# Performance work log

Measured on AMD Instinct MI355X. Metric: run time of the kernel, lower is better.

The kernel has to match this reference:

```python
import jax, jax.numpy as jnp
import numpy as np

N_NODES = 75000
N_EDGES = 1200000


def gcn_conv(x, src, dst, W, b, n):
    # linear transform first (PyG GCNConv applies lin before propagate)
    h = x @ W  # [n, out]
    # add self loops
    loop = jnp.arange(n, dtype=src.dtype)
    s = jnp.concatenate([src, loop])
    d = jnp.concatenate([dst, loop])
    # symmetric normalization: deg computed on destination after self-loops
    deg = jnp.zeros((n,), dtype=h.dtype).at[d].add(1.0)
    dinv = jnp.where(deg > 0, jax.lax.rsqrt(deg), 0.0)
    norm = dinv[s] * dinv[d]  # [E+n]
    msgs = h[s] * norm[:, None]  # gather + scale, [E+n, out]
    out = jax.ops.segment_sum(msgs, d, num_segments=n)  # scatter-add
    return out + b


def setup_inputs() -> dict:
    key = jax.random.key(0)
    ks = jax.random.split(key, 6)
    x = jax.random.normal(ks[0], (N_NODES, 64), dtype=jnp.float32)
    edge_index = jax.random.randint(ks[1], (2, N_EDGES), 0, N_NODES, dtype=jnp.int64)
    # Glorot-ish scaled weights
    W1 = jax.random.normal(ks[2], (64, 64), dtype=jnp.float32) * (1.0 / np.sqrt(64))
    b1 = jax.random.normal(ks[3], (64,), dtype=jnp.float32) * 0.01
    W2 = jax.random.normal(ks[4], (64, 16), dtype=jnp.float32) * (1.0 / np.sqrt(64))
    b2 = jax.random.normal(ks[5], (16,), dtype=jnp.float32) * 0.01
    return {"x": x, "edge_index": edge_index, "W1": W1, "b1": b1, "W2": W2, "b2": b2}


def reference(x, edge_index, W1, b1, W2, b2):
    src, dst = edge_index[0], edge_index[1]
    h = gcn_conv(x, src, dst, W1, b1, N_NODES)
    h = jax.nn.relu(h)
    # dropout is identity in eval mode
    out = gcn_conv(h, src, dst, W2, b2, N_NODES)
    return out
```

## Files before the change

kernel.cpp:

```cpp
#include <hip/hip_runtime.h>


#define NBSHIFT 9
#define BUCKET_NODES 512
#define CAP 10240
#define CHA 8192
#define TA 512
#define TB 512
#define MAXNB 160
#define EPT 16

__device__ __forceinline__ unsigned bfpack(float a, float b) {
  unsigned ua = __float_as_uint(a), ub = __float_as_uint(b);
  ua += 0x7fffu + ((ua >> 16) & 1u);
  ub += 0x7fffu + ((ub >> 16) & 1u);
  return (ua >> 16) | (ub & 0xffff0000u);
}
__device__ __forceinline__ float bflo(unsigned u) { return __uint_as_float(u << 16); }
__device__ __forceinline__ float bfhi(unsigned u) { return __uint_as_float(u & 0xffff0000u); }

__launch_bounds__(TA)
__global__ void kA_bucket(const int* __restrict__ src, const int* __restrict__ dst,
                          int* __restrict__ bucketCur, int* __restrict__ bucketArr,
                          int NB, int E) {
  __shared__ int stage[CHA];
  __shared__ unsigned char binOf[CHA];
  __shared__ int cnt[MAXNB];
  __shared__ int off[MAXNB];
  __shared__ int gpos[MAXNB];
  __shared__ int cursor[MAXNB];
  __shared__ int scanbuf[256];
  int t = threadIdx.x;
  int e0 = blockIdx.x * CHA;

  for (int i = t; i < NB; i += TA) cnt[i] = 0;
  __syncthreads();
  int dreg[EPT];
  #pragma unroll
  for (int j = 0; j < EPT; j++) {
    int e = e0 + t + j * TA;
    dreg[j] = (e < E) ? dst[e] : -1;
    if (dreg[j] >= 0) atomicAdd(&cnt[dreg[j] >> NBSHIFT], 1);
  }
  __syncthreads();
  if (t < 256) scanbuf[t] = (t < NB) ? cnt[t] : 0;
  __syncthreads();
  for (int o = 1; o < 256; o <<= 1) {
    int add = (t < 256 && t >= o) ? scanbuf[t - o] : 0;
    __syncthreads();
    if (t < 256) scanbuf[t] += add;
    __syncthreads();
  }
  if (t < NB) {
    off[t] = scanbuf[t] - cnt[t];
    cursor[t] = off[t];
    gpos[t] = (cnt[t] > 0) ? atomicAdd(&bucketCur[t], cnt[t]) : 0;
  }
  __syncthreads();
  #pragma unroll
  for (int j = 0; j < EPT; j++) {
    int e = e0 + t + j * TA;
    if (dreg[j] >= 0) {
      int d = dreg[j], s = src[e];
      int b = d >> NBSHIFT;
      int p = atomicAdd(&cursor[b], 1);
      stage[p] = (s << NBSHIFT) | (d & (BUCKET_NODES - 1));
      binOf[p] = (unsigned char)b;
    }
  }
  __syncthreads();
  int total = scanbuf[255];
  for (int i = t; i < total; i += TA) {
    int b = binOf[i];
    int destIdx = gpos[b] + (i - off[b]);
    if (destIdx < CAP) bucketArr[b * CAP + destIdx] = stage[i];
  }
}

__launch_bounds__(TB)
__global__ void kB_fill(const int* __restrict__ bucketArr, const int* __restrict__ bucketCur,
                        int* __restrict__ rp, float* __restrict__ dinv,
                        int* __restrict__ col, int N, int NB) {
  __shared__ int cnts[MAXNB];
  __shared__ int hist[BUCKET_NODES];
  __shared__ int cur[BUCKET_NODES];
  __shared__ int wsum[8], woff[8];
  __shared__ int s_base;
  int b = blockIdx.x;
  int t = threadIdx.x;
  int nE = min(bucketCur[b], CAP);
  int base = b * CAP;

  if (t < NB) cnts[t] = min(bucketCur[t], CAP);
  hist[t] = 0;
  __syncthreads();
  for (int i = t; i < nE; i += TB)
    atomicAdd(&hist[bucketArr[base + i] & (BUCKET_NODES - 1)], 1);
  __syncthreads();
  int myv = hist[t];
  int lane = t & 63, w = t >> 6;
  int incl = myv;
  #pragma unroll
  for (int o = 1; o < 64; o <<= 1) {
    int v = __shfl_up(incl, o);
    if (lane >= o) incl += v;
  }
  if (lane == 63) wsum[w] = incl;
  __syncthreads();
  if (t == 0) {
    int acc = 0;
    for (int i = 0; i < b; i++) acc += cnts[i];
    s_base = acc;
    int a2 = 0;
    #pragma unroll
    for (int i = 0; i < 8; i++) { woff[i] = a2; a2 += wsum[i]; }
    if (b == NB - 1) rp[N] = acc + nE;
  }
  __syncthreads();
  int gexcl = s_base + woff[w] + (incl - myv);
  cur[t] = gexcl;
  int gnode = b * BUCKET_NODES + t;
  if (gnode < N) {
    rp[gnode] = gexcl;
    dinv[gnode] = rsqrtf((float)(myv + 1));
  }
  __syncthreads();
  for (int i = t; i < nE; i += TB) {
    int v = bucketArr[base + i];
    int p = atomicAdd(&cur[v & (BUCKET_NODES - 1)], 1);
    col[p] = v >> NBSHIFT;
  }
}

__launch_bounds__(256)
__global__ void k_gemm64(const float4* __restrict__ X4, const float4* __restrict__ W4,
                         const float* __restrict__ dinv, uint2* __restrict__ outb,
                         int n) {
  __shared__ float4 Xs[64 * 17];
  __shared__ float4 Ws[64 * 16];
  int t = threadIdx.x;
  int base = blockIdx.x * 64;
  {
    int rr = t >> 2, q = t & 3;
    int r = base + rr;
    #pragma unroll
    for (int c = 0; c < 4; c++) {
      float4 v = make_float4(0.f, 0.f, 0.f, 0.f);
      if (r < n) v = X4[r * 16 + q * 4 + c];
      Xs[rr * 17 + q * 4 + c] = v;
      Ws[t + 256 * c] = W4[t + 256 * c];
    }
  }
  __syncthreads();

  int tx = t & 15, ty = t >> 4;
  float4 a0 = make_float4(0.f, 0.f, 0.f, 0.f), a1 = a0, a2 = a0, a3 = a0;
  #pragma unroll
  for (int kb = 0; kb < 16; kb++) {
    float4 x0 = Xs[(ty * 4 + 0) * 17 + kb];
    float4 x1 = Xs[(ty * 4 + 1) * 17 + kb];
    float4 x2 = Xs[(ty * 4 + 2) * 17 + kb];
    float4 x3 = Xs[(ty * 4 + 3) * 17 + kb];
    float4 w0 = Ws[(kb * 4 + 0) * 16 + tx];
    float4 w1 = Ws[(kb * 4 + 1) * 16 + tx];
    float4 w2 = Ws[(kb * 4 + 2) * 16 + tx];
    float4 w3 = Ws[(kb * 4 + 3) * 16 + tx];
    #define FMA4(A, XS) \
      A.x = fmaf(XS.x, w0.x, A.x); A.y = fmaf(XS.x, w0.y, A.y); \
      A.z = fmaf(XS.x, w0.z, A.z); A.w = fmaf(XS.x, w0.w, A.w); \
      A.x = fmaf(XS.y, w1.x, A.x); A.y = fmaf(XS.y, w1.y, A.y); \
      A.z = fmaf(XS.y, w1.z, A.z); A.w = fmaf(XS.y, w1.w, A.w); \
      A.x = fmaf(XS.z, w2.x, A.x); A.y = fmaf(XS.z, w2.y, A.y); \
      A.z = fmaf(XS.z, w2.z, A.z); A.w = fmaf(XS.z, w2.w, A.w); \
      A.x = fmaf(XS.w, w3.x, A.x); A.y = fmaf(XS.w, w3.y, A.y); \
      A.z = fmaf(XS.w, w3.z, A.z); A.w = fmaf(XS.w, w3.w, A.w);
    FMA4(a0, x0) FMA4(a1, x1) FMA4(a2, x2) FMA4(a3, x3)
    #undef FMA4
  }
  #pragma unroll
  for (int i = 0; i < 4; i++) {
    int r = base + ty * 4 + i;
    if (r < n) {
      float s = dinv[r];
      float4 a = (i == 0) ? a0 : (i == 1) ? a1 : (i == 2) ? a2 : a3;
      uint2 pk;
      pk.x = bfpack(a.x * s, a.y * s);
      pk.y = bfpack(a.z * s, a.w * s);
      outb[r * 16 + tx] = pk;
    }
  }
}

__launch_bounds__(256)
__global__ void k_agg64(const uint2* __restrict__ hsb,
                        const int* __restrict__ rp,
                        const int* __restrict__ col,
                        const float* __restrict__ dinv,
                        const float* __restrict__ b1,
                        uint2* __restrict__ h1b,
                        int n) {
  int lane = threadIdx.x & 63;
  int c = lane & 15;
  int node = ((blockIdx.x * blockDim.x + threadIdx.x) >> 6) * 4 + (lane >> 4);
  if (node >= n) return;

  float4 b14 = ((const float4*)b1)[c];
  int s0 = rp[node], s1 = rp[node + 1];
  int dt = s1 - s0 + 1;
  float ax = 0.f, ay = 0.f, az = 0.f, aw = 0.f;
  int t = 0;
  int i0 = 0, i1 = 0, i2 = 0, i3 = 0, i4 = 0, i5 = 0, i6 = 0, i7 = 0;
  i0 = node;
  if (1 < dt) i1 = col[s0 + 0];
  if (2 < dt) i2 = col[s0 + 1];
  if (3 < dt) i3 = col[s0 + 2];
  if (4 < dt) i4 = col[s0 + 3];
  if (5 < dt) i5 = col[s0 + 4];
  if (6 < dt) i6 = col[s0 + 5];
  if (7 < dt) i7 = col[s0 + 6];
  while (t < dt) {
    int c0 = i0, c1 = i1, c2 = i2, c3 = i3, c4 = i4, c5 = i5, c6 = i6, c7 = i7;
    bool h1_ = (t + 1) < dt, h2_ = (t + 2) < dt, h3_ = (t + 3) < dt;
    bool h4_ = (t + 4) < dt, h5_ = (t + 5) < dt, h6_ = (t + 6) < dt;
    bool h7_ = (t + 7) < dt;
    int tn = t + 8;
    if (tn + 0 < dt) i0 = col[s0 + tn - 1];
    if (tn + 1 < dt) i1 = col[s0 + tn + 0];
    if (tn + 2 < dt) i2 = col[s0 + tn + 1];
    if (tn + 3 < dt) i3 = col[s0 + tn + 2];
    if (tn + 4 < dt) i4 = col[s0 + tn + 3];
    if (tn + 5 < dt) i5 = col[s0 + tn + 4];
    if (tn + 6 < dt) i6 = col[s0 + tn + 5];
    if (tn + 7 < dt) i7 = col[s0 + tn + 6];
    uint2 u0 = hsb[c0 * 16 + c];
    uint2 u1 = h1_ ? hsb[c1 * 16 + c] : make_uint2(0u, 0u);
    uint2 u2 = h2_ ? hsb[c2 * 16 + c] : make_uint2(0u, 0u);
    uint2 u3 = h3_ ? hsb[c3 * 16 + c] : make_uint2(0u, 0u);
    uint2 u4 = h4_ ? hsb[c4 * 16 + c] : make_uint2(0u, 0u);
    uint2 u5 = h5_ ? hsb[c5 * 16 + c] : make_uint2(0u, 0u);
    uint2 u6 = h6_ ? hsb[c6 * 16 + c] : make_uint2(0u, 0u);
    uint2 u7 = h7_ ? hsb[c7 * 16 + c] : make_uint2(0u, 0u);
    #define ACC(U) \
      ax += bflo(U.x); ay += bfhi(U.x); az += bflo(U.y); aw += bfhi(U.y);
    ACC(u0) ACC(u1) ACC(u2) ACC(u3) ACC(u4) ACC(u5) ACC(u6) ACC(u7)
    #undef ACC
    t = tn;
  }
  float dv = dinv[node];
  uint2 pk;
  pk.x = bfpack(fmaxf(ax * dv + b14.x, 0.f), fmaxf(ay * dv + b14.y, 0.f));
  pk.y = bfpack(fmaxf(az * dv + b14.z, 0.f), fmaxf(aw * dv + b14.w, 0.f));
  h1b[node * 16 + c] = pk;
}

__launch_bounds__(256)
__global__ void k_gemmB(const uint2* __restrict__ h1b,
                        const float4* __restrict__ W24,
                        const float* __restrict__ dinv,
                        unsigned* __restrict__ hs2b,
                        int n) {
  __shared__ float4 Ws[256];
  int t = threadIdx.x;
  Ws[t] = W24[t];
  __syncthreads();
  int tx = t & 3, ty = t >> 2;
  int r0 = blockIdx.x * 256 + ty * 4;
  float4 a0 = make_float4(0.f, 0.f, 0.f, 0.f), a1 = a0, a2 = a0, a3 = a0;
  #pragma unroll
  for (int q = 0; q < 16; q++) {
    uint2 u0 = (r0 + 0 < n) ? h1b[(r0 + 0) * 16 + q] : make_uint2(0u, 0u);
    uint2 u1 = (r0 + 1 < n) ? h1b[(r0 + 1) * 16 + q] : make_uint2(0u, 0u);
    uint2 u2 = (r0 + 2 < n) ? h1b[(r0 + 2) * 16 + q] : make_uint2(0u, 0u);
    uint2 u3 = (r0 + 3 < n) ? h1b[(r0 + 3) * 16 + q] : make_uint2(0u, 0u);
    #pragma unroll
    for (int kk = 0; kk < 4; kk++) {
      float4 w = Ws[(4 * q + kk) * 4 + tx];
      float v0 = (kk == 0) ? bflo(u0.x) : (kk == 1) ? bfhi(u0.x) : (kk == 2) ? bflo(u0.y) : bfhi(u0.y);
      float v1 = (kk == 0) ? bflo(u1.x) : (kk == 1) ? bfhi(u1.x) : (kk == 2) ? bflo(u1.y) : bfhi(u1.y);
      float v2 = (kk == 0) ? bflo(u2.x) : (kk == 1) ? bfhi(u2.x) : (kk == 2) ? bflo(u2.y) : bfhi(u2.y);
      float v3 = (kk == 0) ? bflo(u3.x) : (kk == 1) ? bfhi(u3.x) : (kk == 2) ? bflo(u3.y) : bfhi(u3.y);
      a0.x = fmaf(v0, w.x, a0.x); a0.y = fmaf(v0, w.y, a0.y);
      a0.z = fmaf(v0, w.z, a0.z); a0.w = fmaf(v0, w.w, a0.w);
      a1.x = fmaf(v1, w.x, a1.x); a1.y = fmaf(v1, w.y, a1.y);
      a1.z = fmaf(v1, w.z, a1.z); a1.w = fmaf(v1, w.w, a1.w);
      a2.x = fmaf(v2, w.x, a2.x); a2.y = fmaf(v2, w.y, a2.y);
      a2.z = fmaf(v2, w.z, a2.z); a2.w = fmaf(v2, w.w, a2.w);
      a3.x = fmaf(v3, w.x, a3.x); a3.y = fmaf(v3, w.y, a3.y);
      a3.z = fmaf(v3, w.z, a3.z); a3.w = fmaf(v3, w.w, a3.w);
    }
  }
  #pragma unroll
  for (int i = 0; i < 4; i++) {
    int r = r0 + i;
    if (r < n) {
      float dv = dinv[r];
      float4 a = (i == 0) ? a0 : (i == 1) ? a1 : (i == 2) ? a2 : a3;
      hs2b[r * 8 + 2 * tx]     = bfpack(a.x * dv, a.y * dv);
      hs2b[r * 8 + 2 * tx + 1] = bfpack(a.z * dv, a.w * dv);
    }
  }
}

__launch_bounds__(256)
__global__ void k_agg16(const uint2* __restrict__ hs2b,
                        const int* __restrict__ rp,
                        const int* __restrict__ col,
                        const float* __restrict__ dinv,
                        const float* __restrict__ b2,
                        float4* __restrict__ out4,
                        int n) {
  int lane = threadIdx.x & 63;
  int hl = lane & 7;
  int c = hl & 3;
  int sub = hl >> 2;
  int node = ((blockIdx.x * blockDim.x + threadIdx.x) >> 6) * 8 + (lane >> 3);
  if (node >= n) return;

  int s0 = rp[node], s1 = rp[node + 1];
  int dt = s1 - s0 + 1;
  float ax = 0.f, ay = 0.f, az = 0.f, aw = 0.f;
  int t = sub;
  int i0 = 0, i1 = 0, i2 = 0, i3 = 0;
  if (t < dt)     i0 = (t == 0) ? node : col[s0 + t - 1];
  if (t + 2 < dt) i1 = col[s0 + t + 1];
  if (t + 4 < dt) i2 = col[s0 + t + 3];
  if (t + 6 < dt) i3 = col[s0 + t + 5];
  while (t < dt) {
    int c0 = i0, c1 = i1, c2 = i2, c3 = i3;
    bool h1_ = (t + 2) < dt, h2_ = (t + 4) < dt, h3_ = (t + 6) < dt;
    int tn = t + 8;
    if (tn < dt)     i0 = col[s0 + tn - 1];
    if (tn + 2 < dt) i1 = col[s0 + tn + 1];
    if (tn + 4 < dt) i2 = col[s0 + tn + 3];
    if (tn + 6 < dt) i3 = col[s0 + tn + 5];
    uint2 u0 = hs2b[c0 * 4 + c];
    uint2 u1 = h1_ ? hs2b[c1 * 4 + c] : make_uint2(0u, 0u);
    uint2 u2 = h2_ ? hs2b[c2 * 4 + c] : make_uint2(0u, 0u);
    uint2 u3 = h3_ ? hs2b[c3 * 4 + c] : make_uint2(0u, 0u);
    ax += bflo(u0.x) + bflo(u1.x) + bflo(u2.x) + bflo(u3.x);
    ay += bfhi(u0.x) + bfhi(u1.x) + bfhi(u2.x) + bfhi(u3.x);
    az += bflo(u0.y) + bflo(u1.y) + bflo(u2.y) + bflo(u3.y);
    aw += bfhi(u0.y) + bfhi(u1.y) + bfhi(u2.y) + bfhi(u3.y);
    t = tn;
  }
  ax += __shfl_xor(ax, 4);
  ay += __shfl_xor(ay, 4);
  az += __shfl_xor(az, 4);
  aw += __shfl_xor(aw, 4);
  if (sub == 0) {
    float dv = dinv[node];
    float4 b24 = ((const float4*)b2)[c];
    float4 o;
    o.x = ax * dv + b24.x;
    o.y = ay * dv + b24.y;
    o.z = az * dv + b24.z;
    o.w = aw * dv + b24.w;
    out4[node * 4 + c] = o;
  }
}

extern "C" void kernel_launch(void* const* d_in, const int* in_sizes, int n_in,
                              void* d_out, int out_size, void* d_ws, size_t ws_size,
                              hipStream_t stream) {
  const float* x  = (const float*)d_in[0];
  const int* edges = (const int*)d_in[1];
  const float* W1 = (const float*)d_in[2];
  const float* b1 = (const float*)d_in[3];
  const float* W2 = (const float*)d_in[4];
  const float* b2 = (const float*)d_in[5];
  float* out = (float*)d_out;

  const int N = in_sizes[0] / 64;
  const int E = in_sizes[1] / 2;
  const int* src = edges;
  const int* dst = edges + E;
  const int NB = (N + BUCKET_NODES - 1) >> NBSHIFT;

  auto align = [](size_t v) { return (v + 255) & ~(size_t)255; };
  char* p = (char*)d_ws;
  float* dinv       = (float*)p; p += align((size_t)N * 4);
  int*   rp         = (int*)p;   p += align((size_t)(N + 1) * 4);
  int*   bucketCur  = (int*)p;   p += align((size_t)MAXNB * 4);
  int*   col        = (int*)p;   p += align((size_t)E * 4);
  float* hs1        = (float*)p; p += align((size_t)N * 64 * 4);
  float* h1b        = (float*)p; p += align((size_t)N * 64 * 2);
  float* hs2        = (float*)p; p += align((size_t)N * 16 * 2);
  int* bucketArr = (int*)hs1;

  const int nbA = (E + CHA - 1) / CHA;
  const int nbW4 = (int)((((size_t)(N + 3) / 4) * 64 + 255) / 256);
  const int nbW8 = (int)((((size_t)(N + 7) / 8) * 64 + 255) / 256);

  hipMemsetAsync(bucketCur, 0, (size_t)MAXNB * 4, stream);
  kA_bucket<<<nbA, TA, 0, stream>>>(src, dst, bucketCur, bucketArr, NB, E);
  kB_fill  <<<NB, TB, 0, stream>>>(bucketArr, bucketCur, rp, dinv, col, N, NB);

  k_gemm64<<<(N + 63) / 64, 256, 0, stream>>>((const float4*)x, (const float4*)W1,
                                              dinv, (uint2*)hs1, N);
  k_agg64 <<<nbW4, 256, 0, stream>>>((const uint2*)hs1, rp, col, dinv,
                                     b1, (uint2*)h1b, N);
  k_gemmB <<<(N + 255) / 256, 256, 0, stream>>>((const uint2*)h1b,
                                                (const float4*)W2, dinv,
                                                (unsigned*)hs2, N);
  k_agg16 <<<nbW8, 256, 0, stream>>>((const uint2*)hs2, rp, col, dinv,
                                     b2, (float4*)out, N);
}
```

Baseline: 120.5 us.

## Fuse bucketing with layer-1 GEMM and fold W2 GEMM into aggregation

The edge-bucketing kernel and the layer-1 dense transform now run as one launch with a block-index split, so the GEMM no longer depends on dinv and overlaps with graph construction. The source-side dinv scaling moves into the aggregation loop as a per-neighbor gather. The layer-2 GEMM is folded into the layer-1 aggregation via wavefront shuffles, which removes the h1 intermediate round trip and one launch. In exchange the aggregation does extra dinv gathers, bucketArr gets its own workspace region instead of aliasing hs1, and the unscaled bf16 h differs slightly in rounding.

After: 255.4 us. 112% more time.

```diff
diff --git a/kernel.cpp b/kernel.cpp
--- a/kernel.cpp
+++ b/kernel.cpp
@@ -19,61 +19,113 @@
 __device__ __forceinline__ float bflo(unsigned u) { return __uint_as_float(u << 16); }
 __device__ __forceinline__ float bfhi(unsigned u) { return __uint_as_float(u & 0xffff0000u); }
 
-__launch_bounds__(TA)
-__global__ void kA_bucket(const int* __restrict__ src, const int* __restrict__ dst,
-                          int* __restrict__ bucketCur, int* __restrict__ bucketArr,
-                          int NB, int E) {
-  __shared__ int stage[CHA];
-  __shared__ unsigned char binOf[CHA];
-  __shared__ int cnt[MAXNB];
-  __shared__ int off[MAXNB];
-  __shared__ int gpos[MAXNB];
-  __shared__ int cursor[MAXNB];
-  __shared__ int scanbuf[256];
+__launch_bounds__(512)
+__global__ void k_fused1(const int* __restrict__ srcp, const int* __restrict__ dstp,
+                         int* __restrict__ bucketCur, int* __restrict__ bucketArr,
+                         int NB, int E, int nbA,
+                         const float4* __restrict__ X4, const float4* __restrict__ W4,
+                         uint2* __restrict__ outb, int n) {
+  __shared__ __align__(16) char smem[44544];
   int t = threadIdx.x;
-  int e0 = blockIdx.x * CHA;
-
-  for (int i = t; i < NB; i += TA) cnt[i] = 0;
-  __syncthreads();
-  int dreg[EPT];
-  #pragma unroll
-  for (int j = 0; j < EPT; j++) {
-    int e = e0 + t + j * TA;
-    dreg[j] = (e < E) ? dst[e] : -1;
-    if (dreg[j] >= 0) atomicAdd(&cnt[dreg[j] >> NBSHIFT], 1);
-  }
-  __syncthreads();
-  if (t < 256) scanbuf[t] = (t < NB) ? cnt[t] : 0;
-  __syncthreads();
-  for (int o = 1; o < 256; o <<= 1) {
-    int add = (t < 256 && t >= o) ? scanbuf[t - o] : 0;
-    __syncthreads();
-    if (t < 256) scanbuf[t] += add;
-    __syncthreads();
-  }
-  if (t < NB) {
-    off[t] = scanbuf[t] - cnt[t];
-    cursor[t] = off[t];
-    gpos[t] = (cnt[t] > 0) ? atomicAdd(&bucketCur[t], cnt[t]) : 0;
-  }
-  __syncthreads();
-  #pragma unroll
-  for (int j = 0; j < EPT; j++) {
-    int e = e0 + t + j * TA;
-    if (dreg[j] >= 0) {
-      int d = dreg[j], s = src[e];
-      int b = d >> NBSHIFT;
-      int p = atomicAdd(&cursor[b], 1);
-      stage[p] = (s << NBSHIFT) | (d & (BUCKET_NODES - 1));
-      binOf[p] = (unsigned char)b;
-    }
-  }
-  __syncthreads();
-  int total = scanbuf[255];
-  for (int i = t; i < total; i += TA) {
-    int b = binOf[i];
-    int destIdx = gpos[b] + (i - off[b]);
-    if (destIdx < CAP) bucketArr[b * CAP + destIdx] = stage[i];
+  if ((int)blockIdx.x < nbA) {
+    int* stage = (int*)smem;
+    unsigned char* binOf = (unsigned char*)(smem + 32768);
+    int* cnt    = (int*)(smem + 40960);
+    int* off    = (int*)(smem + 41600);
+    int* gpos   = (int*)(smem + 42240);
+    int* cursor = (int*)(smem + 42880);
+    int* scanbuf= (int*)(smem + 43520);
+    int e0 = blockIdx.x * CHA;
+
+    for (int i = t; i < NB; i += TA) cnt[i] = 0;
+    __syncthreads();
+    int dreg[EPT];
+    #pragma unroll
+    for (int j = 0; j < EPT; j++) {
+      int e = e0 + t + j * TA;
+      dreg[j] = (e < E) ? dstp[e] : -1;
+      if (dreg[j] >= 0) atomicAdd(&cnt[dreg[j] >> NBSHIFT], 1);
+    }
+    __syncthreads();
+    if (t < 256) scanbuf[t] = (t < NB) ? cnt[t] : 0;
+    __syncthreads();
+    for (int o = 1; o < 256; o <<= 1) {
+      int add = (t < 256 && t >= o) ? scanbuf[t - o] : 0;
+      __syncthreads();
+      if (t < 256) scanbuf[t] += add;
+      __syncthreads();
+    }
+    if (t < NB) {
+      off[t] = scanbuf[t] - cnt[t];
+      cursor[t] = off[t];
+      gpos[t] = (cnt[t] > 0) ? atomicAdd(&bucketCur[t], cnt[t]) : 0;
+    }
+    __syncthreads();
+    #pragma unroll
+    for (int j = 0; j < EPT; j++) {
+      int e = e0 + t + j * TA;
+      if (dreg[j] >= 0) {
+        int d = dreg[j], s = srcp[e];
+        int b = d >> NBSHIFT;
+        int p = atomicAdd(&cursor[b], 1);
+        stage[p] = (s << NBSHIFT) | (d & (BUCKET_NODES - 1));
+        binOf[p] = (unsigned char)b;
+      }
+    }
+    __syncthreads();
+    int total = scanbuf[255];
+    for (int i = t; i < total; i += TA) {
+      int b = binOf[i];
+      int destIdx = gpos[b] + (i - off[b]);
+      if (destIdx < CAP) bucketArr[b * CAP + destIdx] = stage[i];
+    }
+  } else {
+    float4* Xs = (float4*)smem;
+    float4* Ws = (float4*)(smem + 17408);
+    int base = ((int)blockIdx.x - nbA) * 64;
+    {
+      int rr = t >> 3, q = t & 7;
+      int r = base + rr;
+      float4 z = make_float4(0.f, 0.f, 0.f, 0.f);
+      Xs[rr * 17 + q]     = (r < n) ? X4[r * 16 + q]     : z;
+      Xs[rr * 17 + q + 8] = (r < n) ? X4[r * 16 + q + 8] : z;
+      Ws[t]       = W4[t];
+      Ws[t + 512] = W4[t + 512];
+    }
+    __syncthreads();
+    int tx = t & 15, tyy = t >> 4;
+    float4 a0 = make_float4(0.f, 0.f, 0.f, 0.f), a1 = a0;
+    #pragma unroll
+    for (int kb = 0; kb < 16; kb++) {
+      float4 x0 = Xs[(tyy * 2 + 0) * 17 + kb];
+      float4 x1 = Xs[(tyy * 2 + 1) * 17 + kb];
+      float4 w0 = Ws[(kb * 4 + 0) * 16 + tx];
+      float4 w1 = Ws[(kb * 4 + 1) * 16 + tx];
+      float4 w2 = Ws[(kb * 4 + 2) * 16 + tx];
+      float4 w3 = Ws[(kb * 4 + 3) * 16 + tx];
+      #define FMA4(A, XS) \
+        A.x = fmaf(XS.x, w0.x, A.x); A.y = fmaf(XS.x, w0.y, A.y); \
+        A.z = fmaf(XS.x, w0.z, A.z); A.w = fmaf(XS.x, w0.w, A.w); \
+        A.x = fmaf(XS.y, w1.x, A.x); A.y = fmaf(XS.y, w1.y, A.y); \
+        A.z = fmaf(XS.y, w1.z, A.z); A.w = fmaf(XS.y, w1.w, A.w); \
+        A.x = fmaf(XS.z, w2.x, A.x); A.y = fmaf(XS.z, w2.y, A.y); \
+        A.z = fmaf(XS.z, w2.z, A.z); A.w = fmaf(XS.z, w2.w, A.w); \
+        A.x = fmaf(XS.w, w3.x, A.x); A.y = fmaf(XS.w, w3.y, A.y); \
+        A.z = fmaf(XS.w, w3.z, A.z); A.w = fmaf(XS.w, w3.w, A.w);
+      FMA4(a0, x0) FMA4(a1, x1)
+      #undef FMA4
+    }
+    #pragma unroll
+    for (int i = 0; i < 2; i++) {
+      int r = base + tyy * 2 + i;
+      if (r < n) {
+        float4 a = i ? a1 : a0;
+        uint2 pk;
+        pk.x = bfpack(a.x, a.y);
+        pk.y = bfpack(a.z, a.w);
+        outb[r * 16 + tx] = pk;
+      }
+    }
   }
 }
 
@@ -133,72 +185,17 @@
 }
 
 __launch_bounds__(256)
-__global__ void k_gemm64(const float4* __restrict__ X4, const float4* __restrict__ W4,
-                         const float* __restrict__ dinv, uint2* __restrict__ outb,
-                         int n) {
-  __shared__ float4 Xs[64 * 17];
-  __shared__ float4 Ws[64 * 16];
-  int t = threadIdx.x;
-  int base = blockIdx.x * 64;
-  {
-    int rr = t >> 2, q = t & 3;
-    int r = base + rr;
-    #pragma unroll
-    for (int c = 0; c < 4; c++) {
-      float4 v = make_float4(0.f, 0.f, 0.f, 0.f);
-      if (r < n) v = X4[r * 16 + q * 4 + c];
-      Xs[rr * 17 + q * 4 + c] = v;
-      Ws[t + 256 * c] = W4[t + 256 * c];
-    }
-  }
-  __syncthreads();
-
-  int tx = t & 15, ty = t >> 4;
-  float4 a0 = make_float4(0.f, 0.f, 0.f, 0.f), a1 = a0, a2 = a0, a3 = a0;
-  #pragma unroll
-  for (int kb = 0; kb < 16; kb++) {
-    float4 x0 = Xs[(ty * 4 + 0) * 17 + kb];
-    float4 x1 = Xs[(ty * 4 + 1) * 17 + kb];
-    float4 x2 = Xs[(ty * 4 + 2) * 17 + kb];
-    float4 x3 = Xs[(ty * 4 + 3) * 17 + kb];
-    float4 w0 = Ws[(kb * 4 + 0) * 16 + tx];
-    float4 w1 = Ws[(kb * 4 + 1) * 16 + tx];
-    float4 w2 = Ws[(kb * 4 + 2) * 16 + tx];
-    float4 w3 = Ws[(kb * 4 + 3) * 16 + tx];
-    #define FMA4(A, XS) \
-      A.x = fmaf(XS.x, w0.x, A.x); A.y = fmaf(XS.x, w0.y, A.y); \
-      A.z = fmaf(XS.x, w0.z, A.z); A.w = fmaf(XS.x, w0.w, A.w); \
-      A.x = fmaf(XS.y, w1.x, A.x); A.y = fmaf(XS.y, w1.y, A.y); \
-      A.z = fmaf(XS.y, w1.z, A.z); A.w = fmaf(XS.y, w1.w, A.w); \
-      A.x = fmaf(XS.z, w2.x, A.x); A.y = fmaf(XS.z, w2.y, A.y); \
-      A.z = fmaf(XS.z, w2.z, A.z); A.w = fmaf(XS.z, w2.w, A.w); \
-      A.x = fmaf(XS.w, w3.x, A.x); A.y = fmaf(XS.w, w3.y, A.y); \
-      A.z = fmaf(XS.w, w3.z, A.z); A.w = fmaf(XS.w, w3.w, A.w);
-    FMA4(a0, x0) FMA4(a1, x1) FMA4(a2, x2) FMA4(a3, x3)
-    #undef FMA4
-  }
-  #pragma unroll
-  for (int i = 0; i < 4; i++) {
-    int r = base + ty * 4 + i;
-    if (r < n) {
-      float s = dinv[r];
-      float4 a = (i == 0) ? a0 : (i == 1) ? a1 : (i == 2) ? a2 : a3;
-      uint2 pk;
-      pk.x = bfpack(a.x * s, a.y * s);
-      pk.y = bfpack(a.z * s, a.w * s);
-      outb[r * 16 + tx] = pk;
-    }
-  }
-}
-
-__launch_bounds__(256)
-__global__ void k_agg64(const uint2* __restrict__ hsb,
+__global__ void k_aggW2(const uint2* __restrict__ hsb,
                         const int* __restrict__ rp,
                         const int* __restrict__ col,
                         const float* __restrict__ dinv,
                         const float* __restrict__ b1,
-                        uint2* __restrict__ h1b,
+                        const float* __restrict__ W2,
+                        unsigned* __restrict__ hs2b,
                         int n) {
+  __shared__ float W2s[1024];
+  for (int i = threadIdx.x; i < 1024; i += 256) W2s[i] = W2[i];
+  __syncthreads();
   int lane = threadIdx.x & 63;
   int c = lane & 15;
   int node = ((blockIdx.x * blockDim.x + threadIdx.x) >> 6) * 4 + (lane >> 4);
@@ -209,8 +206,7 @@
   int dt = s1 - s0 + 1;
   float ax = 0.f, ay = 0.f, az = 0.f, aw = 0.f;
   int t = 0;
-  int i0 = 0, i1 = 0, i2 = 0, i3 = 0, i4 = 0, i5 = 0, i6 = 0, i7 = 0;
-  i0 = node;
+  int i0 = node, i1 = 0, i2 = 0, i3 = 0, i4 = 0, i5 = 0, i6 = 0, i7 = 0;
   if (1 < dt) i1 = col[s0 + 0];
   if (2 < dt) i2 = col[s0 + 1];
   if (3 < dt) i3 = col[s0 + 2];
@@ -232,6 +228,8 @@
     if (tn + 5 < dt) i5 = col[s0 + tn + 4];
     if (tn + 6 < dt) i6 = col[s0 + tn + 5];
     if (tn + 7 < dt) i7 = col[s0 + tn + 6];
+    float d0 = dinv[c0], d1 = dinv[c1], d2 = dinv[c2], d3 = dinv[c3];
+    float d4 = dinv[c4], d5 = dinv[c5], d6 = dinv[c6], d7 = dinv[c7];
     uint2 u0 = hsb[c0 * 16 + c];
     uint2 u1 = h1_ ? hsb[c1 * 16 + c] : make_uint2(0u, 0u);
     uint2 u2 = h2_ ? hsb[c2 * 16 + c] : make_uint2(0u, 0u);
@@ -240,65 +238,37 @@
     uint2 u5 = h5_ ? hsb[c5 * 16 + c] : make_uint2(0u, 0u);
     uint2 u6 = h6_ ? hsb[c6 * 16 + c] : make_uint2(0u, 0u);
     uint2 u7 = h7_ ? hsb[c7 * 16 + c] : make_uint2(0u, 0u);
-    #define ACC(U) \
-      ax += bflo(U.x); ay += bfhi(U.x); az += bflo(U.y); aw += bfhi(U.y);
-    ACC(u0) ACC(u1) ACC(u2) ACC(u3) ACC(u4) ACC(u5) ACC(u6) ACC(u7)
+    #define ACC(U, D) \
+      ax = fmaf(D, bflo(U.x), ax); ay = fmaf(D, bfhi(U.x), ay); \
+      az = fmaf(D, bflo(U.y), az); aw = fmaf(D, bfhi(U.y), aw);
+    ACC(u0, d0) ACC(u1, d1) ACC(u2, d2) ACC(u3, d3)
+    ACC(u4, d4) ACC(u5, d5) ACC(u6, d6) ACC(u7, d7)
     #undef ACC
     t = tn;
   }
   float dv = dinv[node];
-  uint2 pk;
-  pk.x = bfpack(fmaxf(ax * dv + b14.x, 0.f), fmaxf(ay * dv + b14.y, 0.f));
-  pk.y = bfpack(fmaxf(az * dv + b14.z, 0.f), fmaxf(aw * dv + b14.w, 0.f));
-  h1b[node * 16 + c] = pk;
-}
-
-__launch_bounds__(256)
-__global__ void k_gemmB(const uint2* __restrict__ h1b,
-                        const float4* __restrict__ W24,
-                        const float* __restrict__ dinv,
-                        unsigned* __restrict__ hs2b,
-                        int n) {
-  __shared__ float4 Ws[256];
-  int t = threadIdx.x;
-  Ws[t] = W24[t];
-  __syncthreads();
-  int tx = t & 3, ty = t >> 2;
-  int r0 = blockIdx.x * 256 + ty * 4;
-  float4 a0 = make_float4(0.f, 0.f, 0.f, 0.f), a1 = a0, a2 = a0, a3 = a0;
+  float h0  = fmaxf(ax * dv + b14.x, 0.f);
+  float h1v = fmaxf(ay * dv + b14.y, 0.f);
+  float h2v = fmaxf(az * dv + b14.z, 0.f);
+  float h3v = fmaxf(aw * dv + b14.w, 0.f);
+
+  float val = 0.f;
+  int gb = lane & 48;
   #pragma unroll
-  for (int q = 0; q < 16; q++) {
-    uint2 u0 = (r0 + 0 < n) ? h1b[(r0 + 0) * 16 + q] : make_uint2(0u, 0u);
-    uint2 u1 = (r0 + 1 < n) ? h1b[(r0 + 1) * 16 + q] : make_uint2(0u, 0u);
-    uint2 u2 = (r0 + 2 < n) ? h1b[(r0 + 2) * 16 + q] : make_uint2(0u, 0u);
-    uint2 u3 = (r0 + 3 < n) ? h1b[(r0 + 3) * 16 + q] : make_uint2(0u, 0u);
-    #pragma unroll
-    for (int kk = 0; kk < 4; kk++) {
-      float4 w = Ws[(4 * q + kk) * 4 + tx];
-      float v0 = (kk == 0) ? bflo(u0.x) : (kk == 1) ? bfhi(u0.x) : (kk == 2) ? bflo(u0.y) : bfhi(u0.y);
-      float v1 = (kk == 0) ? bflo(u1.x) : (kk == 1) ? bfhi(u1.x) : (kk == 2) ? bflo(u1.y) : bfhi(u1.y);
-      float v2 = (kk == 0) ? bflo(u2.x) : (kk == 1) ? bfhi(u2.x) : (kk == 2) ? bflo(u2.y) : bfhi(u2.y);
-      float v3 = (kk == 0) ? bflo(u3.x) : (kk == 1) ? bfhi(u3.x) : (kk == 2) ? bflo(u3.y) : bfhi(u3.y);
-      a0.x = fmaf(v0, w.x, a0.x); a0.y = fmaf(v0, w.y, a0.y);
-      a0.z = fmaf(v0, w.z, a0.z); a0.w = fmaf(v0, w.w, a0.w);
-      a1.x = fmaf(v1, w.x, a1.x); a1.y = fmaf(v1, w.y, a1.y);
-      a1.z = fmaf(v1, w.z, a1.z); a1.w = fmaf(v1, w.w, a1.w);
-      a2.x = fmaf(v2, w.x, a2.x); a2.y = fmaf(v2, w.y, a2.y);
-      a2.z = fmaf(v2, w.z, a2.z); a2.w = fmaf(v2, w.w, a2.w);
-      a3.x = fmaf(v3, w.x, a3.x); a3.y = fmaf(v3, w.y, a3.y);
-      a3.z = fmaf(v3, w.z, a3.z); a3.w = fmaf(v3, w.w, a3.w);
-    }
-  }
-  #pragma unroll
-  for (int i = 0; i < 4; i++) {
-    int r = r0 + i;
-    if (r < n) {
-      float dv = dinv[r];
-      float4 a = (i == 0) ? a0 : (i == 1) ? a1 : (i == 2) ? a2 : a3;
-      hs2b[r * 8 + 2 * tx]     = bfpack(a.x * dv, a.y * dv);
-      hs2b[r * 8 + 2 * tx + 1] = bfpack(a.z * dv, a.w * dv);
-    }
-  }
+  for (int kq = 0; kq < 16; kq++) {
+    int srcl = gb + kq;
+    float v0 = __shfl(h0, srcl);
+    float v1 = __shfl(h1v, srcl);
+    float v2 = __shfl(h2v, srcl);
+    float v3 = __shfl(h3v, srcl);
+    val = fmaf(v0, W2s[(4 * kq + 0) * 16 + c], val);
+    val = fmaf(v1, W2s[(4 * kq + 1) * 16 + c], val);
+    val = fmaf(v2, W2s[(4 * kq + 2) * 16 + c], val);
+    val = fmaf(v3, W2s[(4 * kq + 3) * 16 + c], val);
+  }
+  val *= dv;
+  float vnext = __shfl_down(val, 1);
+  if ((c & 1) == 0) hs2b[node * 8 + (c >> 1)] = bfpack(val, vnext);
 }
 
 __launch_bounds__(256)
@@ -382,26 +352,23 @@
   int*   rp         = (int*)p;   p += align((size_t)(N + 1) * 4);
   int*   bucketCur  = (int*)p;   p += align((size_t)MAXNB * 4);
   int*   col        = (int*)p;   p += align((size_t)E * 4);
-  float* hs1        = (float*)p; p += align((size_t)N * 64 * 4);
-  float* h1b        = (float*)p; p += align((size_t)N * 64 * 2);
+  int*   bucketArr  = (int*)p;   p += align((size_t)MAXNB * CAP * 4);
+  float* hs1        = (float*)p; p += align((size_t)N * 64 * 2);
   float* hs2        = (float*)p; p += align((size_t)N * 16 * 2);
-  int* bucketArr = (int*)hs1;
 
   const int nbA = (E + CHA - 1) / CHA;
+  const int ngemm = (N + 63) / 64;
   const int nbW4 = (int)((((size_t)(N + 3) / 4) * 64 + 255) / 256);
   const int nbW8 = (int)((((size_t)(N + 7) / 8) * 64 + 255) / 256);
 
   hipMemsetAsync(bucketCur, 0, (size_t)MAXNB * 4, stream);
-  kA_bucket<<<nbA, TA, 0, stream>>>(src, dst, bucketCur, bucketArr, NB, E);
-  kB_fill  <<<NB, TB, 0, stream>>>(bucketArr, bucketCur, rp, dinv, col, N, NB);
-
-  k_gemm64<<<(N + 63) / 64, 256, 0, stream>>>((const float4*)x, (const float4*)W1,
-                                              dinv, (uint2*)hs1, N);
-  k_agg64 <<<nbW4, 256, 0, stream>>>((const uint2*)hs1, rp, col, dinv,
-                                     b1, (uint2*)h1b, N);
-  k_gemmB <<<(N + 255) / 256, 256, 0, stream>>>((const uint2*)h1b,
-                                                (const float4*)W2, dinv,
-                                                (unsigned*)hs2, N);
-  k_agg16 <<<nbW8, 256, 0, stream>>>((const uint2*)hs2, rp, col, dinv,
-                                     b2, (float4*)out, N);
-}
+  k_fused1<<<nbA + ngemm, 512, 0, stream>>>(src, dst, bucketCur, bucketArr,
+                                            NB, E, nbA,
+                                            (const float4*)x, (const float4*)W1,
+                                            (uint2*)hs1, N);
+  kB_fill<<<NB, TB, 0, stream>>>(bucketArr, bucketCur, rp, dinv, col, N, NB);
+  k_aggW2<<<nbW4, 256, 0, stream>>>((const uint2*)hs1, rp, col, dinv,
+                                    b1, W2, (unsigned*)hs2, N);
+  k_agg16<<<nbW8, 256, 0, stream>>>((const uint2*)hs2, rp, col, dinv,
+                                    b2, (float4*)out, N);
+}
```

## Fuse layer-2 linear transform into layer-1 aggregation via warp shuffles

Applied to the files above, without the earlier changes.

Merges the layer-1 aggregation kernel with the separate 64x16 GEMM. Each 16-lane group holds its node's 64-wide ReLU output, and the W2 product is formed with cross-lane shuffles against W2 staged in shared memory. This removes one kernel launch and the bf16 h1 intermediate write and re-read. The cost is 64 shuffles and 64 LDS reads per lane in the aggregation kernel, plus a 4KB W2 load and a block barrier in every block.

Result: faster. 117.2 us, median of 2 (-2.7%).

```diff
diff --git a/kernel.cpp b/kernel.cpp
--- a/kernel.cpp
+++ b/kernel.cpp
@@ -192,13 +192,17 @@
 }
 
 __launch_bounds__(256)
-__global__ void k_agg64(const uint2* __restrict__ hsb,
+__global__ void k_aggW2(const uint2* __restrict__ hsb,
                         const int* __restrict__ rp,
                         const int* __restrict__ col,
                         const float* __restrict__ dinv,
                         const float* __restrict__ b1,
-                        uint2* __restrict__ h1b,
+                        const float* __restrict__ W2,
+                        unsigned* __restrict__ hs2b,
                         int n) {
+  __shared__ float W2s[1024];
+  for (int i = threadIdx.x; i < 1024; i += 256) W2s[i] = W2[i];
+  __syncthreads();
   int lane = threadIdx.x & 63;
   int c = lane & 15;
   int node = ((blockIdx.x * blockDim.x + threadIdx.x) >> 6) * 4 + (lane >> 4);
@@ -209,8 +213,7 @@
   int dt = s1 - s0 + 1;
   float ax = 0.f, ay = 0.f, az = 0.f, aw = 0.f;
   int t = 0;
-  int i0 = 0, i1 = 0, i2 = 0, i3 = 0, i4 = 0, i5 = 0, i6 = 0, i7 = 0;
-  i0 = node;
+  int i0 = node, i1 = 0, i2 = 0, i3 = 0, i4 = 0, i5 = 0, i6 = 0, i7 = 0;
   if (1 < dt) i1 = col[s0 + 0];
   if (2 < dt) i2 = col[s0 + 1];
   if (3 < dt) i3 = col[s0 + 2];
@@ -247,58 +250,28 @@
     t = tn;
   }
   float dv = dinv[node];
-  uint2 pk;
-  pk.x = bfpack(fmaxf(ax * dv + b14.x, 0.f), fmaxf(ay * dv + b14.y, 0.f));
-  pk.y = bfpack(fmaxf(az * dv + b14.z, 0.f), fmaxf(aw * dv + b14.w, 0.f));
-  h1b[node * 16 + c] = pk;
-}
-
-__launch_bounds__(256)
-__global__ void k_gemmB(const uint2* __restrict__ h1b,
-                        const float4* __restrict__ W24,
-                        const float* __restrict__ dinv,
-                        unsigned* __restrict__ hs2b,
-                        int n) {
-  __shared__ float4 Ws[256];
-  int t = threadIdx.x;
-  Ws[t] = W24[t];
-  __syncthreads();
-  int tx = t & 3, ty = t >> 2;
-  int r0 = blockIdx.x * 256 + ty * 4;
-  float4 a0 = make_float4(0.f, 0.f, 0.f, 0.f), a1 = a0, a2 = a0, a3 = a0;
-  #pragma unroll
-  for (int q = 0; q < 16; q++) {
-    uint2 u0 = (r0 + 0 < n) ? h1b[(r0 + 0) * 16 + q] : make_uint2(0u, 0u);
-    uint2 u1 = (r0 + 1 < n) ? h1b[(r0 + 1) * 16 + q] : make_uint2(0u, 0u);
-    uint2 u2 = (r0 + 2 < n) ? h1b[(r0 + 2) * 16 + q] : make_uint2(0u, 0u);
-    uint2 u3 = (r0 + 3 < n) ? h1b[(r0 + 3) * 16 + q] : make_uint2(0u, 0u);
-    #pragma unroll
-    for (int kk = 0; kk < 4; kk++) {
-      float4 w = Ws[(4 * q + kk) * 4 + tx];
-      float v0 = (kk == 0) ? bflo(u0.x) : (kk == 1) ? bfhi(u0.x) : (kk == 2) ? bflo(u0.y) : bfhi(u0.y);
-      float v1 = (kk == 0) ? bflo(u1.x) : (kk == 1) ? bfhi(u1.x) : (kk == 2) ? bflo(u1.y) : bfhi(u1.y);
-      float v2 = (kk == 0) ? bflo(u2.x) : (kk == 1) ? bfhi(u2.x) : (kk == 2) ? bflo(u2.y) : bfhi(u2.y);
-      float v3 = (kk == 0) ? bflo(u3.x) : (kk == 1) ? bfhi(u3.x) : (kk == 2) ? bflo(u3.y) : bfhi(u3.y);
-      a0.x = fmaf(v0, w.x, a0.x); a0.y = fmaf(v0, w.y, a0.y);
-      a0.z = fmaf(v0, w.z, a0.z); a0.w = fmaf(v0, w.w, a0.w);
-      a1.x = fmaf(v1, w.x, a1.x); a1.y = fmaf(v1, w.y, a1.y);
-      a1.z = fmaf(v1, w.z, a1.z); a1.w = fmaf(v1, w.w, a1.w);
-      a2.x = fmaf(v2, w.x, a2.x); a2.y = fmaf(v2, w.y, a2.y);
-      a2.z = fmaf(v2, w.z, a2.z); a2.w = fmaf(v2, w.w, a2.w);
-      a3.x = fmaf(v3, w.x, a3.x); a3.y = fmaf(v3, w.y, a3.y);
-      a3.z = fmaf(v3, w.z, a3.z); a3.w = fmaf(v3, w.w, a3.w);
-    }
-  }
-  #pragma unroll
-  for (int i = 0; i < 4; i++) {
-    int r = r0 + i;
-    if (r < n) {
-      float dv = dinv[r];
-      float4 a = (i == 0) ? a0 : (i == 1) ? a1 : (i == 2) ? a2 : a3;
-      hs2b[r * 8 + 2 * tx]     = bfpack(a.x * dv, a.y * dv);
-      hs2b[r * 8 + 2 * tx + 1] = bfpack(a.z * dv, a.w * dv);
-    }
-  }
+  float h0  = fmaxf(ax * dv + b14.x, 0.f);
+  float h1v = fmaxf(ay * dv + b14.y, 0.f);
+  float h2v = fmaxf(az * dv + b14.z, 0.f);
+  float h3v = fmaxf(aw * dv + b14.w, 0.f);
+
+  float val = 0.f;
+  int gb = lane & 48;
+  #pragma unroll
+  for (int kq = 0; kq < 16; kq++) {
+    int srcl = gb + kq;
+    float v0 = __shfl(h0, srcl);
+    float v1 = __shfl(h1v, srcl);
+    float v2 = __shfl(h2v, srcl);
+    float v3 = __shfl(h3v, srcl);
+    val = fmaf(v0, W2s[(4 * kq + 0) * 16 + c], val);
+    val = fmaf(v1, W2s[(4 * kq + 1) * 16 + c], val);
+    val = fmaf(v2, W2s[(4 * kq + 2) * 16 + c], val);
+    val = fmaf(v3, W2s[(4 * kq + 3) * 16 + c], val);
+  }
+  val *= dv;
+  float vnext = __shfl_down(val, 1);
+  if ((c & 1) == 0) hs2b[node * 8 + (c >> 1)] = bfpack(val, vnext);
 }
 
 __launch_bounds__(256)
@@ -383,7 +356,6 @@
   int*   bucketCur  = (int*)p;   p += align((size_t)MAXNB * 4);
   int*   col        = (int*)p;   p += align((size_t)E * 4);
   float* hs1        = (float*)p; p += align((size_t)N * 64 * 4);
-  float* h1b        = (float*)p; p += align((size_t)N * 64 * 2);
   float* hs2        = (float*)p; p += align((size_t)N * 16 * 2);
   int* bucketArr = (int*)hs1;
 
@@ -397,11 +369,8 @@
 
   k_gemm64<<<(N + 63) / 64, 256, 0, stream>>>((const float4*)x, (const float4*)W1,
                                               dinv, (uint2*)hs1, N);
-  k_agg64 <<<nbW4, 256, 0, stream>>>((const uint2*)hs1, rp, col, dinv,
-                                     b1, (uint2*)h1b, N);
-  k_gemmB <<<(N + 255) / 256, 256, 0, stream>>>((const uint2*)h1b,
-                                                (const float4*)W2, dinv,
-                                                (unsigned*)hs2, N);
+  k_aggW2 <<<nbW4, 256, 0, stream>>>((const uint2*)hs1, rp, col, dinv,
+                                     b1, W2, (unsigned*)hs2, N);
   k_agg16 <<<nbW8, 256, 0, stream>>>((const uint2*)hs2, rp, col, dinv,
                                      b2, (float4*)out, N);
 }
```
